# Kernel optimization log

Measured on AMD Instinct MI355X. Metric: run time of the kernel, lower is better.

## Reference

```python
import jax, jax.numpy as jnp
import numpy as np

B, T, V, D, H, DK = 64, 384, 12, 256, 4, 64

def _ln(x, g, b):
    m = jnp.mean(x, -1, keepdims=True)
    v = jnp.var(x, -1, keepdims=True)
    return (x - m) * jax.lax.rsqrt(v + 1e-5) * g + b

def _grn(x, W1, b1, W2, b2, Wg, bg, lng, lnb, ctx=None, Wc=None, Ws=None, bs=None):
    # eta2 = ELU(fc1(x) + ctx_proj(ctx)); eta1 = fc2(eta2); GLU; residual; LN
    h = x @ W1 + b1
    if ctx is not None:
        h = h + ctx @ Wc
    h = jax.nn.elu(h)
    h = h @ W2 + b2
    g = h @ Wg + bg
    a, gate = jnp.split(g, 2, axis=-1)
    gated = a * jax.nn.sigmoid(gate)
    skip = x if Ws is None else x @ Ws + bs
    return _ln(skip + gated, lng, lnb)

def setup_inputs() -> dict:
    key = jax.random.key(0)
    ks = iter(jax.random.split(key, 48))
    def rn(shape, s=0.02):
        return jax.random.normal(next(ks), shape, jnp.float32) * s
    return {
        'x': jax.random.normal(next(ks), (B, T, V, D), jnp.float32),
        'context': jax.random.normal(next(ks), (B, D), jnp.float32),
        # flattened GRN of VSN: in=V*D, hidden=D, out=V, context=D, skip needed
        'fg_W1': rn((V * D, D)), 'fg_b1': jnp.zeros((D,), jnp.float32),
        'fg_Wc': rn((D, D)),
        'fg_W2': rn((D, D)), 'fg_b2': jnp.zeros((D,), jnp.float32),
        'fg_Wg': rn((D, 2 * V)), 'fg_bg': jnp.zeros((2 * V,), jnp.float32),
        'fg_Ws': rn((V * D, V)), 'fg_bs': jnp.zeros((V,), jnp.float32),
        'fg_lng': jnp.ones((V,), jnp.float32), 'fg_lnb': jnp.zeros((V,), jnp.float32),
        # per-variable GRNs (V of them, in=out=hidden=D, no skip/ctx), stacked
        'sv_W1': rn((V, D, D)), 'sv_b1': jnp.zeros((V, D), jnp.float32),
        'sv_W2': rn((V, D, D)), 'sv_b2': jnp.zeros((V, D), jnp.float32),
        'sv_Wg': rn((V, D, 2 * D)), 'sv_bg': jnp.zeros((V, 2 * D), jnp.float32),
        'sv_lng': jnp.ones((V, D), jnp.float32), 'sv_lnb': jnp.zeros((V, D), jnp.float32),
        # static enrichment GRN: in=out=hidden=D with context
        'en_W1': rn((D, D)), 'en_b1': jnp.zeros((D,), jnp.float32),
        'en_Wc': rn((D, D)),
        'en_W2': rn((D, D)), 'en_b2': jnp.zeros((D,), jnp.float32),
        'en_Wg': rn((D, 2 * D)), 'en_bg': jnp.zeros((2 * D,), jnp.float32),
        'en_lng': jnp.ones((D,), jnp.float32), 'en_lnb': jnp.zeros((D,), jnp.float32),
        # interpretable MHA: per-head Q/K, shared V, output proj
        'Wq': rn((H, D, DK)), 'Wk': rn((H, D, DK)),
        'Wv': rn((D, DK)), 'Wo': rn((DK, D)),
    }

def reference(x, context, fg_W1, fg_b1, fg_Wc, fg_W2, fg_b2, fg_Wg, fg_bg, fg_Ws, fg_bs,
              fg_lng, fg_lnb, sv_W1, sv_b1, sv_W2, sv_b2, sv_Wg, sv_bg, sv_lng, sv_lnb,
              en_W1, en_b1, en_Wc, en_W2, en_b2, en_Wg, en_bg, en_lng, en_lnb,
              Wq, Wk, Wv, Wo):
    b, t, v, d = x.shape
    ctx3 = context[:, None, :]  # broadcast static context over time
    # ---- Variable Selection Network ----
    xf = x.reshape(b, t, v * d)
    w = _grn(xf, fg_W1, fg_b1, fg_W2, fg_b2, fg_Wg, fg_bg, fg_lng, fg_lnb,
             ctx=ctx3, Wc=fg_Wc, Ws=fg_Ws, bs=fg_bs)
    w = jax.nn.softmax(w, axis=-1)  # (b,t,v)
    per_var = jax.vmap(_grn, in_axes=(2, 0, 0, 0, 0, 0, 0, 0, 0), out_axes=2)(
        x, sv_W1, sv_b1, sv_W2, sv_b2, sv_Wg, sv_bg, sv_lng, sv_lnb)  # (b,t,v,d)
    sel = jnp.sum(per_var * w[..., None], axis=2)  # (b,t,d)
    # ---- static enrichment GRN ----
    enr = _grn(sel, en_W1, en_b1, en_W2, en_b2, en_Wg, en_bg, en_lng, en_lnb,
               ctx=ctx3, Wc=en_Wc)
    # ---- interpretable multi-head attention (causal), per-head Q/K, shared V ----
    q = jnp.einsum('btd,hdk->hbtk', enr, Wq)
    k = jnp.einsum('btd,hdk->hbtk', enr, Wk)
    vp = enr @ Wv  # (b,t,dk), shared across heads
    scale = jax.lax.rsqrt(jnp.asarray(DK, jnp.float32))
    scores = jnp.einsum('hbqd,hbkd->hbqk', q, k) * scale
    mask = jnp.triu(jnp.ones((t, t), bool), 1)  # True = masked (future)
    scores = jnp.where(mask, jnp.asarray(-1e9, scores.dtype), scores)
    attn = jax.nn.softmax(scores, axis=-1)
    heads = jnp.einsum('hbqk,bkd->hbqd', attn, vp)
    out = jnp.mean(heads, axis=0) @ Wo  # mean over heads then shared output proj
    return out
```

## Files before the change

kernel.cpp:

```cpp
#include <hip/hip_runtime.h>
#include <hip/hip_bf16.h>
#include <stdint.h>
#include <stddef.h>

typedef __bf16 bf16;
typedef __bf16 bf16x8 __attribute__((ext_vector_type(8)));
typedef float  f32x4  __attribute__((ext_vector_type(4)));

#define BTR 24576
#define EPI_BIAS  1
#define EPI_CVEC  2
#define EPI_ELU   4
#define EPI_ATTN  8
#define EPI_GATE  32
#define EPI_PERM  64

__device__ __forceinline__ int perm512(int n) {
  return (n < 256) ? (((n >> 4) << 5) + (n & 15))
                   : ((((n - 256) >> 4) << 5) + ((n - 256) & 15) + 16);
}

template<int EPI, bool AF32, bool CF32>
__global__ __launch_bounds__(256, 2)
void gemm_kernel(const void* __restrict__ Av, int lda, long sAh, long sAb,
                 const bf16* __restrict__ Bt, int ldb, long sBh, long sBb,
                 void* __restrict__ Cv, int ldc, long sC,
                 int K, int zdiv,
                 const float* __restrict__ bias, const float* __restrict__ cvec,
                 long sBias)
{
  __shared__ __align__(16) bf16 As[128 * 32];
  __shared__ __align__(16) bf16 Bs[128 * 32];

  const int tid  = threadIdx.x;
  const int wave = tid >> 6, lane = tid & 63;
  const int wr = wave >> 1, wc = wave & 1;
  const int quad = lane >> 4, l16 = lane & 15;

  const int z  = blockIdx.z;
  const int hh = z / zdiv, bb = z % zdiv;
  const float* AbF = nullptr; const bf16* AbH = nullptr;
  if constexpr (AF32) AbF = (const float*)Av + (long)hh * sAh + (long)bb * sAb;
  else                AbH = (const bf16*)Av  + (long)hh * sAh + (long)bb * sAb;
  const bf16* Bb = Bt + (long)hh * sBh + (long)bb * sBb;
  float* CbF = nullptr; bf16* CbH = nullptr;
  if constexpr (CF32) CbF = (float*)Cv + (long)z * sC;
  else                CbH = (bf16*)Cv  + (long)z * sC;

  const int rowBase = blockIdx.y * 128;
  const int colBase = blockIdx.x * 128;

  f32x4 acc[4][4];
#pragma unroll
  for (int i = 0; i < 4; ++i)
#pragma unroll
    for (int j = 0; j < 4; ++j) { acc[i][j][0]=0.f; acc[i][j][1]=0.f; acc[i][j][2]=0.f; acc[i][j][3]=0.f; }

  const int r0 = tid >> 2, kc = tid & 3;
  const int r1 = tid >> 1, kh = (tid & 1) * 16;
  const int arow = (wr * 64 + l16) * 32 + quad * 8;
  const int brow = (wc * 64 + l16) * 32 + quad * 8;

  f32x4 pf0, pf1, pf2, pf3;
  bf16x8 pa0, pa1, pb0, pb1;
  if constexpr (AF32) {
    const float* p = AbF + (size_t)(rowBase + r1) * lda + kh;
    pf0 = *(const f32x4*)(p);     pf1 = *(const f32x4*)(p + 4);
    pf2 = *(const f32x4*)(p + 8); pf3 = *(const f32x4*)(p + 12);
  } else {
    pa0 = *(const bf16x8*)(AbH + (size_t)(rowBase + r0)      * lda + kc * 8);
    pa1 = *(const bf16x8*)(AbH + (size_t)(rowBase + 64 + r0) * lda + kc * 8);
  }
  pb0 = *(const bf16x8*)(Bb + (size_t)(colBase + r0)      * ldb + kc * 8);
  pb1 = *(const bf16x8*)(Bb + (size_t)(colBase + 64 + r0) * ldb + kc * 8);

  for (int k0 = 0; k0 < K; k0 += 32) {
    __syncthreads();
    if constexpr (AF32) {
      bf16x8 a0, a1;
#pragma unroll
      for (int e = 0; e < 4; ++e) {
        a0[e] = (bf16)pf0[e]; a0[4 + e] = (bf16)pf1[e];
        a1[e] = (bf16)pf2[e]; a1[4 + e] = (bf16)pf3[e];
      }
      *(bf16x8*)(As + r1 * 32 + kh)     = a0;
      *(bf16x8*)(As + r1 * 32 + kh + 8) = a1;
    } else {
      *(bf16x8*)(As +        r0 * 32 + kc * 8) = pa0;
      *(bf16x8*)(As + 2048 + r0 * 32 + kc * 8) = pa1;
    }
    *(bf16x8*)(Bs +        r0 * 32 + kc * 8) = pb0;
    *(bf16x8*)(Bs + 2048 + r0 * 32 + kc * 8) = pb1;
    __syncthreads();

    const int k1 = k0 + 32;
    if (k1 < K) {
      if constexpr (AF32) {
        const float* p = AbF + (size_t)(rowBase + r1) * lda + k1 + kh;
        pf0 = *(const f32x4*)(p);     pf1 = *(const f32x4*)(p + 4);
        pf2 = *(const f32x4*)(p + 8); pf3 = *(const f32x4*)(p + 12);
      } else {
        pa0 = *(const bf16x8*)(AbH + (size_t)(rowBase + r0)      * lda + k1 + kc * 8);
        pa1 = *(const bf16x8*)(AbH + (size_t)(rowBase + 64 + r0) * lda + k1 + kc * 8);
      }
      pb0 = *(const bf16x8*)(Bb + (size_t)(colBase + r0)      * ldb + k1 + kc * 8);
      pb1 = *(const bf16x8*)(Bb + (size_t)(colBase + 64 + r0) * ldb + k1 + kc * 8);
    }

    bf16x8 af[4], bfv[4];
#pragma unroll
    for (int mi = 0; mi < 4; ++mi) af[mi]  = *(const bf16x8*)(As + arow + mi * 512);
#pragma unroll
    for (int ni = 0; ni < 4; ++ni) bfv[ni] = *(const bf16x8*)(Bs + brow + ni * 512);
#pragma unroll
    for (int mi = 0; mi < 4; ++mi)
#pragma unroll
      for (int ni = 0; ni < 4; ++ni)
        acc[mi][ni] = __builtin_amdgcn_mfma_f32_16x16x32_bf16(af[mi], bfv[ni], acc[mi][ni], 0, 0, 0);
  }

  if constexpr (EPI & EPI_GATE) {
    const float* bp = bias + (size_t)z * sBias;
#pragma unroll
    for (int mi = 0; mi < 4; ++mi) {
#pragma unroll
      for (int nj = 0; nj < 2; ++nj) {
        const int ni = nj * 2;
        const int pa = colBase + wc * 64 + ni * 16 + l16;
        const int j  = (colBase >> 1) + wc * 32 + nj * 16 + l16;
        const float ba = bp[pa], bg = bp[pa + 16];
        const int row0 = rowBase + wr * 64 + mi * 16 + quad * 4;
#pragma unroll
        for (int r = 0; r < 4; ++r) {
          float a = acc[mi][ni][r]     + ba;
          float g = acc[mi][ni + 1][r] + bg;
          CbH[(size_t)(row0 + r) * ldc + j] = (bf16)(a / (1.f + __expf(-g)));
        }
      }
    }
    return;
  }
  const int bctx = (EPI & EPI_CVEC) ? (rowBase / 384) : 0;
  const float* bp = (EPI & EPI_BIAS) ? bias + (size_t)z * sBias : nullptr;
#pragma unroll
  for (int mi = 0; mi < 4; ++mi) {
#pragma unroll
    for (int ni = 0; ni < 4; ++ni) {
      const int row0 = rowBase + wr * 64 + mi * 16 + quad * 4;
      const int col  = colBase + wc * 64 + ni * 16 + l16;
      float bv = (EPI & EPI_BIAS) ? bp[col] : 0.f;
      float cv = (EPI & EPI_CVEC) ? cvec[bctx * 256 + col] : 0.f;
#pragma unroll
      for (int r = 0; r < 4; ++r) {
        float v = acc[mi][ni][r] + bv + cv;
        if (EPI & EPI_ELU)  v = v > 0.f ? v : __expf(v) - 1.f;
        if (EPI & EPI_ATTN) { v *= 0.125f; if (col > row0 + r) v = -1e9f; }
        int srow = row0 + r;
        if constexpr (EPI & EPI_PERM) srow = perm512(srow);
        if constexpr (CF32) CbF[(size_t)srow * ldc + col] = v;
        else                CbH[(size_t)srow * ldc + col] = (bf16)v;
      }
    }
  }
}

__global__ __launch_bounds__(256, 2)
void fgwide_kernel(const float* __restrict__ A, const bf16* __restrict__ Bt,
                   bf16* __restrict__ C, const float* __restrict__ bias,
                   const float* __restrict__ cvec)
{
  __shared__ __align__(16) bf16 As[64 * 32];
  __shared__ __align__(16) bf16 Bs[384 * 32];
  const int tid = threadIdx.x;
  const int wave = tid >> 6, lane = tid & 63;
  const int quad = lane >> 4, l16 = lane & 15;
  const int rowBase = blockIdx.x * 64;

  f32x4 acc[4][6];
#pragma unroll
  for (int i = 0; i < 4; ++i)
#pragma unroll
    for (int j = 0; j < 6; ++j) { acc[i][j][0]=0.f; acc[i][j][1]=0.f; acc[i][j][2]=0.f; acc[i][j][3]=0.f; }

  const int r1 = tid >> 2, kh = (tid & 3) * 8;
  const int arow = l16 * 32 + quad * 8;
  const int brow = (wave * 96 + l16) * 32 + quad * 8;

  f32x4 pf0, pf1;
  bf16x8 pbv[6];
  {
    const float* p = A + (size_t)(rowBase + r1) * 3072 + kh;
    pf0 = *(const f32x4*)(p); pf1 = *(const f32x4*)(p + 4);
#pragma unroll
    for (int c = 0; c < 6; ++c) {
      const int idx = c * 256 + tid, rb = idx >> 2, kc2 = idx & 3;
      pbv[c] = *(const bf16x8*)(Bt + (size_t)rb * 3072 + kc2 * 8);
    }
  }
  for (int k0 = 0; k0 < 3072; k0 += 32) {
    __syncthreads();
    bf16x8 av;
#pragma unroll
    for (int e = 0; e < 4; ++e) { av[e] = (bf16)pf0[e]; av[4 + e] = (bf16)pf1[e]; }
    *(bf16x8*)(As + r1 * 32 + kh) = av;
#pragma unroll
    for (int c = 0; c < 6; ++c) {
      const int idx = c * 256 + tid, rb = idx >> 2, kc2 = idx & 3;
      *(bf16x8*)(Bs + rb * 32 + kc2 * 8) = pbv[c];
    }
    __syncthreads();

    const int k1 = k0 + 32;
    if (k1 < 3072) {
      const float* p = A + (size_t)(rowBase + r1) * 3072 + k1 + kh;
      pf0 = *(const f32x4*)(p); pf1 = *(const f32x4*)(p + 4);
#pragma unroll
      for (int c = 0; c < 6; ++c) {
        const int idx = c * 256 + tid, rb = idx >> 2, kc2 = idx & 3;
        pbv[c] = *(const bf16x8*)(Bt + (size_t)rb * 3072 + k1 + kc2 * 8);
      }
    }

    bf16x8 af[4], bfv[6];
#pragma unroll
    for (int mi = 0; mi < 4; ++mi) af[mi]  = *(const bf16x8*)(As + arow + mi * 512);
#pragma unroll
    for (int ni = 0; ni < 6; ++ni) bfv[ni] = *(const bf16x8*)(Bs + brow + ni * 512);
#pragma unroll
    for (int mi = 0; mi < 4; ++mi)
#pragma unroll
      for (int ni = 0; ni < 6; ++ni)
        acc[mi][ni] = __builtin_amdgcn_mfma_f32_16x16x32_bf16(af[mi], bfv[ni], acc[mi][ni], 0, 0, 0);
  }

  const int bctx = rowBase / 384;
#pragma unroll
  for (int mi = 0; mi < 4; ++mi) {
#pragma unroll
    for (int ni = 0; ni < 6; ++ni) {
      const int col = wave * 96 + ni * 16 + l16;
      const bool act = (wave * 96 + ni * 16) < 256;
      const float bv = bias[col];
      const float cv = act ? cvec[bctx * 256 + col] : 0.f;
      const int row0 = rowBase + mi * 16 + quad * 4;
#pragma unroll
      for (int r = 0; r < 4; ++r) {
        float v = acc[mi][ni][r] + bv + cv;
        if (act) v = v > 0.f ? v : __expf(v) - 1.f;
        C[(size_t)(row0 + r) * 384 + col] = (bf16)v;
      }
    }
  }
}

__global__ void prep_kernel(
    const float* fgW1, const float* fgWs, const float* fgW2, const float* fgWg,
    const float* fgb1, const float* fgbs,
    const float* svW1, const float* svWg, const float* svW2,
    const float* enW1, const float* enWg, const float* enW2,
    const float* Wq, const float* Wk, const float* Wv, const float* Wo,
    bf16* fgW1WsT, bf16* fgWgPT, bf16* fgW2C, float* bias384,
    bf16* svW1T, bf16* svWgT, bf16* svW2C,
    bf16* enW1T, bf16* enWgT, bf16* enW2C,
    bf16* WqkvT, bf16* WoT)
{
  long i = (long)blockIdx.x * 256 + threadIdx.x;
  if (i < 1179648) {
    int n = i / 3072, k = i % 3072; float v;
    if (n < 256) v = fgW1[(size_t)k * 256 + n];
    else { int nn = n - 256; v = (nn < 12) ? fgWs[(size_t)k * 12 + nn] : 0.f; }
    fgW1WsT[i] = (bf16)v; return; } i -= 1179648;
  if (i < 32768)  { int n = i >> 8, k = i & 255; fgWgPT[i] = (n < 24) ? (bf16)fgWg[k * 24 + n] : (bf16)0.f; return; } i -= 32768;
  if (i < 65536)  { fgW2C[i] = (bf16)fgW2[i]; return; } i -= 65536;
  if (i < 384)    { bias384[i] = (i < 256) ? fgb1[i] : ((i < 268) ? fgbs[i - 256] : 0.f); return; } i -= 384;
  if (i < 786432) { long v = i >> 16, r = i & 65535; int n = r >> 8, k = r & 255; svW1T[i] = (bf16)svW1[(v << 16) + k * 256 + n]; return; } i -= 786432;
  if (i < 1572864){ long v = i >> 17, r = i & 131071; int n = r >> 8, k = r & 255; svWgT[i] = (bf16)svWg[(v << 17) + k * 512 + n]; return; } i -= 1572864;
  if (i < 786432) { svW2C[i] = (bf16)svW2[i]; return; } i -= 786432;
  if (i < 65536)  { int n = i >> 8, k = i & 255; enW1T[i] = (bf16)enW1[k * 256 + n]; return; } i -= 65536;
  if (i < 131072) { int n = i >> 8, k = i & 255; enWgT[i] = (bf16)enWg[k * 512 + n]; return; } i -= 131072;
  if (i < 65536)  { enW2C[i] = (bf16)enW2[i]; return; } i -= 65536;
  if (i < 163840) { int n = i >> 8, k = i & 255; float val;
                    if (n < 256)      val = Wq[(n >> 6) * 16384 + k * 64 + (n & 63)];
                    else if (n < 512) { int nn = n - 256; val = Wk[(nn >> 6) * 16384 + k * 64 + (nn & 63)]; }
                    else if (n < 576) val = Wv[k * 64 + (n - 512)];
                    else              val = 0.f;
                    WqkvT[i] = (bf16)val; return; } i -= 163840;
  if (i < 16384)  { int n = i >> 6, k = i & 63; WoT[i] = (bf16)Wo[k * 256 + n]; }
}

__global__ void biasfuse_kernel(const float* fgb2, const float* fgWg, const float* fgbg,
                                const float* svb2, const float* svWg, const float* svbg,
                                const float* enb2, const float* enWg, const float* enbg,
                                float* fgBF, float* svBFP, float* enBFP)
{
  int i = blockIdx.x * 256 + threadIdx.x;
  if (i < 128) {
    float s = 0.f;
    if (i < 24) { s = fgbg[i]; for (int k = 0; k < 256; ++k) s += fgb2[k] * fgWg[k * 24 + i]; }
    fgBF[i] = s; return; } i -= 128;
  if (i < 6144) {
    int v = i >> 9, n = i & 511;
    float s = svbg[v * 512 + n];
    const float* W = svWg + (size_t)v * 131072;
    const float* b2 = svb2 + v * 256;
    for (int k = 0; k < 256; ++k) s += b2[k] * W[k * 512 + n];
    svBFP[v * 512 + perm512(n)] = s; return; } i -= 6144;
  if (i < 512) {
    float s = enbg[i];
    for (int k = 0; k < 256; ++k) s += enb2[k] * enWg[k * 512 + i];
    enBFP[perm512(i)] = s; }
}

__global__ void cvec_kernel(const float* __restrict__ ctx, const float* __restrict__ WcFg,
                            const float* __restrict__ WcEn, float* __restrict__ outFg,
                            float* __restrict__ outEn) {
  int b = blockIdx.x, n = threadIdx.x;
  const float* Wc = blockIdx.y ? WcEn : WcFg;
  float* o = blockIdx.y ? outEn : outFg;
  float acc = 0.f;
  for (int d = 0; d < 256; ++d) acc += ctx[b * 256 + d] * Wc[d * 256 + n];
  o[b * 256 + n] = acc;
}

__global__ void lnsm12_kernel(const bf16* __restrict__ B384, const bf16* __restrict__ GP,
                              const float* __restrict__ lng, const float* __restrict__ lnb,
                              float* __restrict__ w) {
  int r = blockIdx.x * 256 + threadIdx.x;
  if (r >= BTR) return;
  float y[12]; float m = 0.f;
#pragma unroll
  for (int j = 0; j < 12; ++j) {
    float a = (float)GP[(size_t)r * 128 + j];
    float g = (float)GP[(size_t)r * 128 + 12 + j];
    float gated = a / (1.f + __expf(-g));
    y[j] = (float)B384[(size_t)r * 384 + 256 + j] + gated; m += y[j];
  }
  m *= (1.f / 12.f);
  float var = 0.f;
#pragma unroll
  for (int j = 0; j < 12; ++j) { float d = y[j] - m; var += d * d; }
  var *= (1.f / 12.f);
  float rstd = rsqrtf(var + 1e-5f);
  float mx = -1e30f;
#pragma unroll
  for (int j = 0; j < 12; ++j) { y[j] = (y[j] - m) * rstd * lng[j] + lnb[j]; mx = fmaxf(mx, y[j]); }
  float s = 0.f;
#pragma unroll
  for (int j = 0; j < 12; ++j) { y[j] = __expf(y[j] - mx); s += y[j]; }
  float inv = 1.f / s;
#pragma unroll
  for (int j = 0; j < 12; ++j) w[r * 12 + j] = y[j] * inv;
}

__device__ __forceinline__ void block_sum2(float a, float b, float& oa, float& ob) {
#pragma unroll
  for (int o = 32; o; o >>= 1) { a += __shfl_xor(a, o); b += __shfl_xor(b, o); }
  __shared__ float ra[4], rb[4];
  int w = threadIdx.x >> 6;
  if ((threadIdx.x & 63) == 0) { ra[w] = a; rb[w] = b; }
  __syncthreads();
  oa = ra[0] + ra[1] + ra[2] + ra[3];
  ob = rb[0] + rb[1] + rb[2] + rb[3];
  __syncthreads();
}

__global__ __launch_bounds__(256)
void selacc4_kernel(const bf16* __restrict__ GATED, const float* __restrict__ x,
                    const float* __restrict__ w, const float* __restrict__ lng,
                    const float* __restrict__ lnb, float* __restrict__ sel,
                    bf16* __restrict__ selb, int v0, int isFirst, int isLast) {
  int r = blockIdx.x, d = threadIdx.x;
  float acc = isFirst ? 0.f : sel[(size_t)r * 256 + d];
#pragma unroll
  for (int vv = 0; vv < 4; ++vv) {
    int v = v0 + vv;
    float gated = (float)GATED[(size_t)vv * ((size_t)BTR * 256) + (size_t)r * 256 + d];
    float y = x[(size_t)r * 3072 + v * 256 + d] + gated;
    float s1, s2;
    block_sum2(y, y * y, s1, s2);
    float mean = s1 * (1.f / 256.f);
    float var  = s2 * (1.f / 256.f) - mean * mean;
    float val  = (y - mean) * rsqrtf(var + 1e-5f) * lng[v * 256 + d] + lnb[v * 256 + d];
    acc += w[r * 12 + v] * val;
  }
  if (isLast) selb[(size_t)r * 256 + d] = (bf16)acc;
  else        sel[(size_t)r * 256 + d] = acc;
}

__global__ __launch_bounds__(256)
void enrln_kernel(const bf16* __restrict__ GATED, const bf16* __restrict__ skip,
                  const float* __restrict__ lng, const float* __restrict__ lnb,
                  bf16* __restrict__ out) {
  int r = blockIdx.x, d = threadIdx.x;
  float gated = (float)GATED[(size_t)r * 256 + d];
  float y = (float)skip[(size_t)r * 256 + d] + gated;
  float s1, s2;
  block_sum2(y, y * y, s1, s2);
  float mean = s1 * (1.f / 256.f);
  float var = s2 * (1.f / 256.f) - mean * mean;
  float norm = (y - mean) * rsqrtf(var + 1e-5f);
  out[(size_t)r * 256 + d] = (bf16)(norm * lng[d] + lnb[d]);
}

__global__ __launch_bounds__(384)
void softmax_avg_kernel(const bf16* __restrict__ S, bf16* __restrict__ P) {
  const int bq = blockIdx.x;
  const int b = bq / 384, q = bq % 384;
  const int j = threadIdx.x;
  const int w = j >> 6;
  __shared__ float red[6];
  float pb = 0.f;
  for (int h = 0; h < 4; ++h) {
    float s = (float)S[((size_t)((h * 64 + b) * 384 + q)) * 384 + j];
    float m = s;
#pragma unroll
    for (int o = 32; o; o >>= 1) m = fmaxf(m, __shfl_xor(m, o));
    if ((j & 63) == 0) red[w] = m;
    __syncthreads();
    m = fmaxf(fmaxf(fmaxf(red[0], red[1]), fmaxf(red[2], red[3])), fmaxf(red[4], red[5]));
    __syncthreads();
    float e = __expf(s - m);
    float l = e;
#pragma unroll
    for (int o = 32; o; o >>= 1) l += __shfl_xor(l, o);
    if ((j & 63) == 0) red[w] = l;
    __syncthreads();
    l = red[0] + red[1] + red[2] + red[3] + red[4] + red[5];
    __syncthreads();
    pb += e / l;
  }
  P[(size_t)bq * 384 + j] = (bf16)(0.25f * pb);
}

template<int EPI, bool AF32, bool CF32>
static inline void rungemm(hipStream_t s,
    const void* A, int lda, const bf16* Bt, int ldb, void* C, int ldc,
    int M, int N, int K,
    const float* bias = nullptr, const float* cvec = nullptr,
    int Z = 1, int zdiv = 1,
    long sAh = 0, long sAb = 0, long sBh = 0, long sBb = 0, long sC = 0, long sBias = 0)
{
  dim3 grid(N / 128, M / 128, Z);
  gemm_kernel<EPI, AF32, CF32><<<grid, 256, 0, s>>>(A, lda, sAh, sAb, Bt, ldb, sBh, sBb, C, ldc, sC, K, zdiv, bias, cvec, sBias);
}

extern "C" void kernel_launch(void* const* d_in, const int* in_sizes, int n_in,
                              void* d_out, int out_size, void* d_ws, size_t ws_size,
                              hipStream_t stream)
{
  (void)in_sizes; (void)n_in; (void)out_size;
  const float* x      = (const float*)d_in[0];
  const float* ctx    = (const float*)d_in[1];
  const float* fg_W1  = (const float*)d_in[2];
  const float* fg_b1  = (const float*)d_in[3];
  const float* fg_Wc  = (const float*)d_in[4];
  const float* fg_W2  = (const float*)d_in[5];
  const float* fg_b2  = (const float*)d_in[6];
  const float* fg_Wg  = (const float*)d_in[7];
  const float* fg_bg  = (const float*)d_in[8];
  const float* fg_Ws  = (const float*)d_in[9];
  const float* fg_bs  = (const float*)d_in[10];
  const float* fg_lng = (const float*)d_in[11];
  const float* fg_lnb = (const float*)d_in[12];
  const float* sv_W1  = (const float*)d_in[13];
  const float* sv_b1  = (const float*)d_in[14];
  const float* sv_W2  = (const float*)d_in[15];
  const float* sv_b2  = (const float*)d_in[16];
  const float* sv_Wg  = (const float*)d_in[17];
  const float* sv_bg  = (const float*)d_in[18];
  const float* sv_lng = (const float*)d_in[19];
  const float* sv_lnb = (const float*)d_in[20];
  const float* en_W1  = (const float*)d_in[21];
  const float* en_b1  = (const float*)d_in[22];
  const float* en_Wc  = (const float*)d_in[23];
  const float* en_W2  = (const float*)d_in[24];
  const float* en_b2  = (const float*)d_in[25];
  const float* en_Wg  = (const float*)d_in[26];
  const float* en_bg  = (const float*)d_in[27];
  const float* en_lng = (const float*)d_in[28];
  const float* en_lnb = (const float*)d_in[29];
  const float* Wq     = (const float*)d_in[30];
  const float* Wk     = (const float*)d_in[31];
  const float* Wv     = (const float*)d_in[32];
  const float* Wo     = (const float*)d_in[33];

  static constexpr size_t OFF_FGW1WST = 0;
  static constexpr size_t OFF_FGWGPT  = OFF_FGW1WST + 2359296;
  static constexpr size_t OFF_FGW2C   = OFF_FGWGPT  + 65536;
  static constexpr size_t OFF_FGW2GT  = OFF_FGW2C   + 131072;
  static constexpr size_t OFF_BIAS384 = OFF_FGW2GT  + 65536;
  static constexpr size_t OFF_FGBF    = OFF_BIAS384 + 1536;
  static constexpr size_t OFF_SVW1T   = OFF_FGBF    + 512;
  static constexpr size_t OFF_SVWGT   = OFF_SVW1T   + 1572864;
  static constexpr size_t OFF_SVW2C   = OFF_SVWGT   + 3145728;
  static constexpr size_t OFF_SVW2GPT = OFF_SVW2C   + 1572864;
  static constexpr size_t OFF_SVBFP   = OFF_SVW2GPT + 3145728;
  static constexpr size_t OFF_ENW1T   = OFF_SVBFP   + 24576;
  static constexpr size_t OFF_ENWGT   = OFF_ENW1T   + 131072;
  static constexpr size_t OFF_ENW2C   = OFF_ENWGT   + 262144;
  static constexpr size_t OFF_ENW2GPT = OFF_ENW2C   + 131072;
  static constexpr size_t OFF_ENBFP   = OFF_ENW2GPT + 262144;
  static constexpr size_t OFF_WQKVT   = OFF_ENBFP   + 2048;
  static constexpr size_t OFF_WOT     = OFF_WQKVT   + 327680;
  static constexpr size_t OFF_CVECFG  = OFF_WOT     + 32768;
  static constexpr size_t OFF_CVECEN  = OFF_CVECFG  + 65536;
  static constexpr size_t ARENA       = OFF_CVECEN  + 65536;
  static constexpr size_t WS_NEEDED = ARENA + 152174592;

  if (ws_size < WS_NEEDED) return;

  char* ws = (char*)d_ws;
  bf16*  fgW1WsT = (bf16*)(ws + OFF_FGW1WST);
  bf16*  fgWgPT  = (bf16*)(ws + OFF_FGWGPT);
  bf16*  fgW2C   = (bf16*)(ws + OFF_FGW2C);
  bf16*  fgW2gT  = (bf16*)(ws + OFF_FGW2GT);
  float* bias384 = (float*)(ws + OFF_BIAS384);
  float* fgBF    = (float*)(ws + OFF_FGBF);
  bf16*  svW1T   = (bf16*)(ws + OFF_SVW1T);
  bf16*  svWgT   = (bf16*)(ws + OFF_SVWGT);
  bf16*  svW2C   = (bf16*)(ws + OFF_SVW2C);
  bf16*  svW2gPT = (bf16*)(ws + OFF_SVW2GPT);
  float* svBFP   = (float*)(ws + OFF_SVBFP);
  bf16*  enW1T   = (bf16*)(ws + OFF_ENW1T);
  bf16*  enWgT   = (bf16*)(ws + OFF_ENWGT);
  bf16*  enW2C   = (bf16*)(ws + OFF_ENW2C);
  bf16*  enW2gPT = (bf16*)(ws + OFF_ENW2GPT);
  float* enBFP   = (float*)(ws + OFF_ENBFP);
  bf16*  WqkvT   = (bf16*)(ws + OFF_WQKVT);
  bf16*  WoT     = (bf16*)(ws + OFF_WOT);
  float* cvecFg  = (float*)(ws + OFF_CVECFG);
  float* cvecEn  = (float*)(ws + OFF_CVECEN);
  char*  ar      = ws + ARENA;
  float* sel     = (float*)(ar + 0);
  bf16*  selb    = (bf16*)(ar + 25165824);
  float* wbuf    = (float*)(ar + 37748736);
  bf16*  H1G     = (bf16*)(ar + 38928384);
  bf16*  BUF384  = (bf16*)(ar + 38928384);
  bf16*  GPAD    = (bf16*)(ar + 57802752);
  bf16*  H1EN    = (bf16*)(ar + 38928384);
  bf16*  GATED   = (bf16*)(ar + 89260032);
  bf16*  GATEDEN = (bf16*)(ar + 89260032);
  bf16*  enr     = (bf16*)(ar + 139591680);
  bf16*  QKV     = (bf16*)(ar + 0);
  bf16*  Pbar    = (bf16*)(ar + 38928384);
  bf16*  Sbuf    = (bf16*)(ar + 64094208);
  bf16*  UT      = (bf16*)(ar + 64094208);
  float* out     = (float*)d_out;

  prep_kernel<<<19010, 256, 0, stream>>>(fg_W1, fg_Ws, fg_W2, fg_Wg, fg_b1, fg_bs,
                                         sv_W1, sv_Wg, sv_W2, en_W1, en_Wg, en_W2,
                                         Wq, Wk, Wv, Wo,
                                         fgW1WsT, fgWgPT, fgW2C, bias384,
                                         svW1T, svWgT, svW2C, enW1T, enWgT, enW2C,
                                         WqkvT, WoT);
  biasfuse_kernel<<<27, 256, 0, stream>>>(fg_b2, fg_Wg, fg_bg, sv_b2, sv_Wg, sv_bg,
                                          en_b2, en_Wg, en_bg, fgBF, svBFP, enBFP);
  cvec_kernel<<<dim3(64, 2), 256, 0, stream>>>(ctx, fg_Wc, en_Wc, cvecFg, cvecEn);

  rungemm<0,        false, false>(stream, fgWgPT, 256, fgW2C, 256, fgW2gT, 256, 128, 256, 256);
  rungemm<EPI_PERM, false, false>(stream, svWgT, 256, svW2C, 256, svW2gPT, 256, 512, 256, 256,
                                  nullptr, nullptr, 12, 12, 0, 131072, 0, 65536, 131072);
  rungemm<EPI_PERM, false, false>(stream, enWgT, 256, enW2C, 256, enW2gPT, 256, 512, 256, 256);

  fgwide_kernel<<<384, 256, 0, stream>>>(x, fgW1WsT, BUF384, bias384, cvecFg);
  rungemm<EPI_BIAS, false, false>(stream, BUF384, 384, fgW2gT, 256, GPAD, 128, BTR, 128, 256, fgBF);
  lnsm12_kernel<<<96, 256, 0, stream>>>(BUF384, GPAD, fg_lng, fg_lnb, wbuf);

  for (int g = 0; g < 3; ++g) {
    rungemm<EPI_BIAS|EPI_ELU, true, false>(
        stream, x + g * 4 * 256, 3072, svW1T + (size_t)g * 4 * 65536, 256, H1G, 256, BTR, 256, 256,
        sv_b1 + g * 4 * 256, nullptr, 4, 4, 0, 256, 0, 65536, (long)BTR * 256, 256);
    rungemm<EPI_BIAS|EPI_GATE, false, false>(
        stream, H1G, 256, svW2gPT + (size_t)g * 4 * 131072, 256, GATED, 256, BTR, 512, 256,
        svBFP + g * 4 * 512, nullptr, 4, 4, 0, (long)BTR * 256, 0, 131072, (long)BTR * 256, 512);
    selacc4_kernel<<<BTR, 256, 0, stream>>>(GATED, x, wbuf, sv_lng, sv_lnb, sel, selb,
                                            g * 4, g == 0, g == 2);
  }

  rungemm<EPI_BIAS|EPI_CVEC|EPI_ELU, false, false>(stream, selb, 256, enW1T, 256, H1EN, 256, BTR, 256, 256, en_b1, cvecEn);
  rungemm<EPI_BIAS|EPI_GATE, false, false>(stream, H1EN, 256, enW2gPT, 256, GATEDEN, 256, BTR, 512, 256, enBFP);
  enrln_kernel<<<BTR, 256, 0, stream>>>(GATEDEN, selb, en_lng, en_lnb, enr);

  rungemm<0, false, false>(stream, enr, 256, WqkvT, 256, QKV, 640, BTR, 640, 256);
  rungemm<EPI_ATTN, false, false>(stream, QKV, 640, QKV + 256, 640, Sbuf, 384, 384, 384, 64,
                                  nullptr, nullptr, 256, 64, 64, 245760L, 64, 245760L, 147456L);
  softmax_avg_kernel<<<BTR, 384, 0, stream>>>(Sbuf, Pbar);
  rungemm<0, false, false>(stream, WoT, 64, QKV + 512, 640, UT, 384, 256, 384, 64,
                           nullptr, nullptr, 64, 64, 0, 0, 0, 245760L, 98304L);
  rungemm<0, false, true>(stream, Pbar, 384, UT, 384, out, 256, 384, 256, 384,
                          nullptr, nullptr, 64, 1, 147456L, 0, 98304L, 0, 98304L);
}
```

Baseline: 1.357 ms.

## Double-buffer LDS tiles and use direct global-to-LDS loads in GEMM kernels

Converts the shared-memory tiles in the generic GEMM and the wide fused-GRN GEMM to double buffers. bf16 operands now go straight from global memory into LDS with global_load_lds instead of staging through registers. This removes one of the two barriers per K-step and lets loads of the next tile overlap MFMA work on the current one. LDS use doubles, which could reduce occupancy, especially for the fgwide kernel (about 53KB). Correctness relies on the lane-to-LDS address mapping of the direct loads matching the old row-major layout.

```diff
diff --git a/kernel.cpp b/kernel.cpp
--- a/kernel.cpp
+++ b/kernel.cpp
@@ -14,6 +14,12 @@
 #define EPI_ATTN  8
 #define EPI_GATE  32
 #define EPI_PERM  64
+
+typedef const __attribute__((address_space(1))) void gas_void;
+typedef __attribute__((address_space(3))) void sas_void;
+__device__ __forceinline__ void gload16(const void* g, void* s) {
+  __builtin_amdgcn_global_load_lds((gas_void*)g, (sas_void*)s, 16, 0, 0);
+}
 
 __device__ __forceinline__ int perm512(int n) {
   return (n < 256) ? (((n >> 4) << 5) + (n & 15))
@@ -29,8 +35,8 @@
                  const float* __restrict__ bias, const float* __restrict__ cvec,
                  long sBias)
 {
-  __shared__ __align__(16) bf16 As[128 * 32];
-  __shared__ __align__(16) bf16 Bs[128 * 32];
+  __shared__ __align__(16) bf16 As[2][128 * 32];
+  __shared__ __align__(16) bf16 Bs[2][128 * 32];
 
   const int tid  = threadIdx.x;
   const int wave = tid >> 6, lane = tid & 63;
@@ -61,62 +67,78 @@
   const int arow = (wr * 64 + l16) * 32 + quad * 8;
   const int brow = (wc * 64 + l16) * 32 + quad * 8;
 
+  char* AsW = (char*)&As[0][0] + wave * 1024;
+  char* BsW = (char*)&Bs[0][0] + wave * 1024;
+
   f32x4 pf0, pf1, pf2, pf3;
-  bf16x8 pa0, pa1, pb0, pb1;
+  const int nt = K >> 5;
+  int cur = 0;
+
   if constexpr (AF32) {
     const float* p = AbF + (size_t)(rowBase + r1) * lda + kh;
     pf0 = *(const f32x4*)(p);     pf1 = *(const f32x4*)(p + 4);
     pf2 = *(const f32x4*)(p + 8); pf3 = *(const f32x4*)(p + 12);
   } else {
-    pa0 = *(const bf16x8*)(AbH + (size_t)(rowBase + r0)      * lda + kc * 8);
-    pa1 = *(const bf16x8*)(AbH + (size_t)(rowBase + 64 + r0) * lda + kc * 8);
-  }
-  pb0 = *(const bf16x8*)(Bb + (size_t)(colBase + r0)      * ldb + kc * 8);
-  pb1 = *(const bf16x8*)(Bb + (size_t)(colBase + 64 + r0) * ldb + kc * 8);
-
-  for (int k0 = 0; k0 < K; k0 += 32) {
-    __syncthreads();
-    if constexpr (AF32) {
-      bf16x8 a0, a1;
-#pragma unroll
-      for (int e = 0; e < 4; ++e) {
-        a0[e] = (bf16)pf0[e]; a0[4 + e] = (bf16)pf1[e];
-        a1[e] = (bf16)pf2[e]; a1[4 + e] = (bf16)pf3[e];
-      }
-      *(bf16x8*)(As + r1 * 32 + kh)     = a0;
-      *(bf16x8*)(As + r1 * 32 + kh + 8) = a1;
-    } else {
-      *(bf16x8*)(As +        r0 * 32 + kc * 8) = pa0;
-      *(bf16x8*)(As + 2048 + r0 * 32 + kc * 8) = pa1;
-    }
-    *(bf16x8*)(Bs +        r0 * 32 + kc * 8) = pb0;
-    *(bf16x8*)(Bs + 2048 + r0 * 32 + kc * 8) = pb1;
-    __syncthreads();
-
-    const int k1 = k0 + 32;
-    if (k1 < K) {
+    gload16(AbH + (size_t)(rowBase + r0)      * lda + kc * 8, AsW);
+    gload16(AbH + (size_t)(rowBase + 64 + r0) * lda + kc * 8, AsW + 4096);
+  }
+  gload16(Bb + (size_t)(colBase + r0)      * ldb + kc * 8, BsW);
+  gload16(Bb + (size_t)(colBase + 64 + r0) * ldb + kc * 8, BsW + 4096);
+  if constexpr (AF32) {
+    bf16x8 a0, a1;
+#pragma unroll
+    for (int e = 0; e < 4; ++e) {
+      a0[e] = (bf16)pf0[e]; a0[4 + e] = (bf16)pf1[e];
+      a1[e] = (bf16)pf2[e]; a1[4 + e] = (bf16)pf3[e];
+    }
+    *(bf16x8*)(&As[0][0] + r1 * 32 + kh)     = a0;
+    *(bf16x8*)(&As[0][0] + r1 * 32 + kh + 8) = a1;
+  }
+  __syncthreads();
+
+  for (int t = 0; t < nt; ++t) {
+    const int nxt = cur ^ 1;
+    if (t + 1 < nt) {
+      const int k1 = (t + 1) * 32;
       if constexpr (AF32) {
         const float* p = AbF + (size_t)(rowBase + r1) * lda + k1 + kh;
         pf0 = *(const f32x4*)(p);     pf1 = *(const f32x4*)(p + 4);
         pf2 = *(const f32x4*)(p + 8); pf3 = *(const f32x4*)(p + 12);
       } else {
-        pa0 = *(const bf16x8*)(AbH + (size_t)(rowBase + r0)      * lda + k1 + kc * 8);
-        pa1 = *(const bf16x8*)(AbH + (size_t)(rowBase + 64 + r0) * lda + k1 + kc * 8);
+        gload16(AbH + (size_t)(rowBase + r0)      * lda + k1 + kc * 8, AsW + nxt * 8192);
+        gload16(AbH + (size_t)(rowBase + 64 + r0) * lda + k1 + kc * 8, AsW + nxt * 8192 + 4096);
       }
-      pb0 = *(const bf16x8*)(Bb + (size_t)(colBase + r0)      * ldb + k1 + kc * 8);
-      pb1 = *(const bf16x8*)(Bb + (size_t)(colBase + 64 + r0) * ldb + k1 + kc * 8);
-    }
-
+      gload16(Bb + (size_t)(colBase + r0)      * ldb + k1 + kc * 8, BsW + nxt * 8192);
+      gload16(Bb + (size_t)(colBase + 64 + r0) * ldb + k1 + kc * 8, BsW + nxt * 8192 + 4096);
+    }
+
+    const bf16* Asc = &As[cur][0];
+    const bf16* Bsc = &Bs[cur][0];
     bf16x8 af[4], bfv[4];
 #pragma unroll
-    for (int mi = 0; mi < 4; ++mi) af[mi]  = *(const bf16x8*)(As + arow + mi * 512);
-#pragma unroll
-    for (int ni = 0; ni < 4; ++ni) bfv[ni] = *(const bf16x8*)(Bs + brow + ni * 512);
+    for (int mi = 0; mi < 4; ++mi) af[mi]  = *(const bf16x8*)(Asc + arow + mi * 512);
+#pragma unroll
+    for (int ni = 0; ni < 4; ++ni) bfv[ni] = *(const bf16x8*)(Bsc + brow + ni * 512);
 #pragma unroll
     for (int mi = 0; mi < 4; ++mi)
 #pragma unroll
       for (int ni = 0; ni < 4; ++ni)
         acc[mi][ni] = __builtin_amdgcn_mfma_f32_16x16x32_bf16(af[mi], bfv[ni], acc[mi][ni], 0, 0, 0);
+
+    if constexpr (AF32) {
+      if (t + 1 < nt) {
+        bf16x8 a0, a1;
+#pragma unroll
+        for (int e = 0; e < 4; ++e) {
+          a0[e] = (bf16)pf0[e]; a0[4 + e] = (bf16)pf1[e];
+          a1[e] = (bf16)pf2[e]; a1[4 + e] = (bf16)pf3[e];
+        }
+        *(bf16x8*)(&As[nxt][0] + r1 * 32 + kh)     = a0;
+        *(bf16x8*)(&As[nxt][0] + r1 * 32 + kh + 8) = a1;
+      }
+    }
+    __syncthreads();
+    cur = nxt;
   }
 
   if constexpr (EPI & EPI_GATE) {
@@ -169,8 +191,8 @@
                    bf16* __restrict__ C, const float* __restrict__ bias,
                    const float* __restrict__ cvec)
 {
-  __shared__ __align__(16) bf16 As[64 * 32];
-  __shared__ __align__(16) bf16 Bs[384 * 32];
+  __shared__ __align__(16) bf16 As[2][64 * 32];
+  __shared__ __align__(16) bf16 Bs[2][384 * 32];
   const int tid = threadIdx.x;
   const int wave = tid >> 6, lane = tid & 63;
   const int quad = lane >> 4, l16 = lane & 15;
@@ -186,51 +208,60 @@
   const int arow = l16 * 32 + quad * 8;
   const int brow = (wave * 96 + l16) * 32 + quad * 8;
 
+  char* BsW = (char*)&Bs[0][0] + wave * 1024;
+
   f32x4 pf0, pf1;
-  bf16x8 pbv[6];
+  int cur = 0;
+
   {
     const float* p = A + (size_t)(rowBase + r1) * 3072 + kh;
     pf0 = *(const f32x4*)(p); pf1 = *(const f32x4*)(p + 4);
 #pragma unroll
     for (int c = 0; c < 6; ++c) {
       const int idx = c * 256 + tid, rb = idx >> 2, kc2 = idx & 3;
-      pbv[c] = *(const bf16x8*)(Bt + (size_t)rb * 3072 + kc2 * 8);
-    }
-  }
-  for (int k0 = 0; k0 < 3072; k0 += 32) {
-    __syncthreads();
+      gload16(Bt + (size_t)rb * 3072 + kc2 * 8, BsW + c * 4096);
+    }
     bf16x8 av;
 #pragma unroll
     for (int e = 0; e < 4; ++e) { av[e] = (bf16)pf0[e]; av[4 + e] = (bf16)pf1[e]; }
-    *(bf16x8*)(As + r1 * 32 + kh) = av;
-#pragma unroll
-    for (int c = 0; c < 6; ++c) {
-      const int idx = c * 256 + tid, rb = idx >> 2, kc2 = idx & 3;
-      *(bf16x8*)(Bs + rb * 32 + kc2 * 8) = pbv[c];
-    }
-    __syncthreads();
-
-    const int k1 = k0 + 32;
-    if (k1 < 3072) {
+    *(bf16x8*)(&As[0][0] + r1 * 32 + kh) = av;
+  }
+  __syncthreads();
+
+  for (int t = 0; t < 96; ++t) {
+    const int nxt = cur ^ 1;
+    if (t + 1 < 96) {
+      const int k1 = (t + 1) * 32;
       const float* p = A + (size_t)(rowBase + r1) * 3072 + k1 + kh;
       pf0 = *(const f32x4*)(p); pf1 = *(const f32x4*)(p + 4);
 #pragma unroll
       for (int c = 0; c < 6; ++c) {
         const int idx = c * 256 + tid, rb = idx >> 2, kc2 = idx & 3;
-        pbv[c] = *(const bf16x8*)(Bt + (size_t)rb * 3072 + k1 + kc2 * 8);
+        gload16(Bt + (size_t)rb * 3072 + k1 + kc2 * 8, BsW + nxt * 24576 + c * 4096);
       }
     }
 
+    const bf16* Asc = &As[cur][0];
+    const bf16* Bsc = &Bs[cur][0];
     bf16x8 af[4], bfv[6];
 #pragma unroll
-    for (int mi = 0; mi < 4; ++mi) af[mi]  = *(const bf16x8*)(As + arow + mi * 512);
-#pragma unroll
-    for (int ni = 0; ni < 6; ++ni) bfv[ni] = *(const bf16x8*)(Bs + brow + ni * 512);
+    for (int mi = 0; mi < 4; ++mi) af[mi]  = *(const bf16x8*)(Asc + arow + mi * 512);
+#pragma unroll
+    for (int ni = 0; ni < 6; ++ni) bfv[ni] = *(const bf16x8*)(Bsc + brow + ni * 512);
 #pragma unroll
     for (int mi = 0; mi < 4; ++mi)
 #pragma unroll
       for (int ni = 0; ni < 6; ++ni)
         acc[mi][ni] = __builtin_amdgcn_mfma_f32_16x16x32_bf16(af[mi], bfv[ni], acc[mi][ni], 0, 0, 0);
+
+    if (t + 1 < 96) {
+      bf16x8 av;
+#pragma unroll
+      for (int e = 0; e < 4; ++e) { av[e] = (bf16)pf0[e]; av[4 + e] = (bf16)pf1[e]; }
+      *(bf16x8*)(&As[nxt][0] + r1 * 32 + kh) = av;
+    }
+    __syncthreads();
+    cur = nxt;
   }
 
   const int bctx = rowBase / 384;
```

Result: no change. 1.361 ms (+0.3%).
